# Optimization experiments

Hardware: AMD Instinct MI355X
Metric: run time of the kernel (lower is better)

## Reference

```python
import jax, jax.numpy as jnp
import numpy as np

WS = 16
NB = 800
THRESH = 0.05


def setup_inputs() -> dict:
    key = jax.random.key(0)
    k1, k2, k3, k4 = jax.random.split(key, 4)
    tensor_msi = jax.random.uniform(k1, (1, 64, 512, 512), dtype=jnp.float32)
    tensor_he = jax.random.uniform(k2, (1, 3, 512, 512), dtype=jnp.float32)
    i_idx = jax.random.randint(k3, (NB,), 0, 512 - WS, dtype=jnp.int32)
    j_idx = jax.random.randint(k4, (NB,), 0, 512 - WS, dtype=jnp.int32)
    return {
        "tensor_msi": tensor_msi,
        "tensor_he": tensor_he,
        "i_idx": i_idx,
        "j_idx": j_idx,
        "window_size": WS,
        "batch": NB,
    }


def reference(tensor_msi, tensor_he, i_idx, j_idx, window_size, batch):
    u = tensor_msi.shape[1]
    msi = tensor_msi[:, : u // 2]  # only first half of MSI channels is used
    ws = window_size
    p = ws * ws

    def get_patch(x, i, j):
        # x: [1, C, M, N] -> [C, ws*ws]
        c = x.shape[1]
        patch = jax.lax.dynamic_slice(x, (0, 0, i, j), (1, c, ws, ws))
        return patch.reshape(c, p)

    def pdist2(x, mask):
        # pairwise squared L2 distance over positions: D[a,b] = sum_k (x[k,a]-x[k,b])^2
        sq = jnp.sum(x * x, axis=0)  # [p]
        gram = jnp.einsum("kp,kq->pq", x, x)  # [p, p]
        d = sq[:, None] + sq[None, :] - 2.0 * gram
        # zero out rows/cols where the HE patch intensity sum < THRESH
        return d * mask[:, None] * mask[None, :]

    def per_patch(i, j):
        pm = get_patch(msi, i, j)  # [u//2, p]
        ph = get_patch(tensor_he, i, j)  # [3, p]
        # NOTE: original code computes index_zero from MSI then overwrites it
        # with the HE-based one; only the HE mask is applied to both.
        mask = (jnp.sum(ph, axis=0) >= THRESH).astype(pm.dtype)  # [p]
        dm = pdist2(pm, mask)
        dh = jax.lax.stop_gradient(pdist2(ph, mask))  # .detach()
        return jnp.mean(jnp.abs(dm - dh))  # L1Loss mean

    losses = jax.vmap(per_patch)(i_idx, j_idx)  # [batch]
    return jnp.sum(losses) / (batch // 5)
```

## Files before the change

### kernel.cpp

```cpp
#include <hip/hip_runtime.h>
#include <hip/hip_bf16.h>


#define PSZ  256
#define IMG  512
#define IMG2 (IMG * IMG)
#define XSTR 40

typedef __attribute__((ext_vector_type(8))) short short8;
typedef __attribute__((ext_vector_type(4))) float float4v;

static __device__ __forceinline__ unsigned short f2bf(float v) {
    union { __hip_bfloat16 b; unsigned short u; } cv;
    cv.b = __float2bfloat16(v);
    return cv.u;
}
static __device__ __forceinline__ float bf2f(unsigned short u) {
    union { unsigned int u; float f; } cv;
    cv.u = ((unsigned int)u) << 16;
    return cv.f;
}

__global__ __launch_bounds__(256, 4)
void corr_loss_kernel(const float* __restrict__ msi,
                      const float* __restrict__ he,
                      const int* __restrict__ i_idx,
                      const int* __restrict__ j_idx,
                      float* __restrict__ partial)
{
    __shared__ __align__(16) unsigned short xs[PSZ * XSTR];
    __shared__ __align__(16) unsigned short eA[PSZ * 8];
    __shared__ __align__(16) unsigned short eB[PSZ * 8];
    __shared__ float red[4];

    const int b = blockIdx.x;
    const int t = threadIdx.x;
    const int i0 = i_idx[b], j0 = j_idx[b];

    {
        const int r = t >> 4, c = t & 15;
        const float* hp = he + (size_t)(i0 + r) * IMG + (j0 + c);
        const float* mp = msi + (size_t)(i0 + r) * IMG + (j0 + c);

        float h0 = hp[0], h1 = hp[IMG2], h2 = hp[2 * IMG2];
        float v[32];
#pragma unroll
        for (int ch = 0; ch < 32; ++ch) v[ch] = mp[(size_t)ch * IMG2];

        const float mf = (h0 + h1 + h2 >= 0.05f) ? 1.f : 0.f;
        const unsigned short hb0 = f2bf(h0 * mf), hb1 = f2bf(h1 * mf), hb2 = f2bf(h2 * mf);
        const float hr0 = bf2f(hb0), hr1 = bf2f(hb1), hr2 = bf2f(hb2);
        const float sh = hr0 * hr0 + hr1 * hr1 + hr2 * hr2;

        float sm = 0.f;
#pragma unroll
        for (int g = 0; g < 4; ++g) {
            unsigned int pk[4];
#pragma unroll
            for (int k = 0; k < 4; ++k) {
                unsigned short lo = f2bf(v[g * 8 + 2 * k]     * mf);
                unsigned short hi = f2bf(v[g * 8 + 2 * k + 1] * mf);
                float fl = bf2f(lo), fh = bf2f(hi);
                sm = fmaf(fl, fl, sm);
                sm = fmaf(fh, fh, sm);
                pk[k] = (unsigned int)lo | ((unsigned int)hi << 16);
            }
            *(uint4*)&xs[t * XSTR + g * 8] = make_uint4(pk[0], pk[1], pk[2], pk[3]);
        }
        const float s = sm - sh;
        const unsigned short shi = f2bf(s);
        const unsigned short slo = f2bf(s - bf2f(shi));
        const unsigned short mb  = (mf != 0.f) ? (unsigned short)0x3F80 : (unsigned short)0;
        const unsigned short d0  = f2bf(2.f * hr0);
        const unsigned short d1  = f2bf(2.f * hr1);
        const unsigned short d2  = f2bf(2.f * hr2);
        *(uint4*)&eA[t * 8] = make_uint4(
            (unsigned)d0 | ((unsigned)d1 << 16),
            (unsigned)d2 | ((unsigned)shi << 16),
            (unsigned)slo | ((unsigned)mb << 16),
            (unsigned)mb);
        *(uint4*)&eB[t * 8] = make_uint4(
            (unsigned)hb0 | ((unsigned)hb1 << 16),
            (unsigned)hb2 | ((unsigned)mb << 16),
            (unsigned)mb | ((unsigned)shi << 16),
            (unsigned)slo);
    }
    __syncthreads();

    const int lane = t & 63, w = t >> 6;
    const int mrow = lane & 15, quad = lane >> 4;
    const short8 zfrag = {0, 0, 0, 0, 0, 0, 0, 0};

    short8 Am[4], Ah[4];
#pragma unroll
    for (int ii = 0; ii < 4; ++ii) {
        const int ri = ((w << 2) + ii) * 16 + mrow;
        uint4 u = *(const uint4*)&xs[ri * XSTR + (quad << 3)];
        u.x = (u.x ^ 0x80008000u) + 0x00800080u;
        u.y = (u.y ^ 0x80008000u) + 0x00800080u;
        u.z = (u.z ^ 0x80008000u) + 0x00800080u;
        u.w = (u.w ^ 0x80008000u) + 0x00800080u;
        Am[ii] = *(const short8*)&u;
        Ah[ii] = (quad == 0) ? *(const short8*)&eA[ri << 3] : zfrag;
    }

    float acc[4] = {0.f, 0.f, 0.f, 0.f};
#pragma unroll 4
    for (int j = 0; j < 16; ++j) {
        const int cj = (j << 4) + mrow;
        short8 Bm = *(const short8*)&xs[cj * XSTR + (quad << 3)];
        short8 Bh = (quad == 0) ? *(const short8*)&eB[cj << 3] : zfrag;
        float4v g[4];
#pragma unroll
        for (int ii = 0; ii < 4; ++ii) {
            g[ii] = (float4v){0.f, 0.f, 0.f, 0.f};
            g[ii] = __builtin_amdgcn_mfma_f32_16x16x32_bf16(Ah[ii], Bh, g[ii], 0, 0, 0);
            g[ii] = __builtin_amdgcn_mfma_f32_16x16x32_bf16(Am[ii], Bm, g[ii], 0, 0, 0);
        }
#pragma unroll
        for (int ii = 0; ii < 4; ++ii) {
            acc[ii] += fabsf(g[ii][0]);
            acc[ii] += fabsf(g[ii][1]);
            acc[ii] += fabsf(g[ii][2]);
            acc[ii] += fabsf(g[ii][3]);
        }
    }
    float a = (acc[0] + acc[1]) + (acc[2] + acc[3]);

#pragma unroll
    for (int off = 32; off > 0; off >>= 1)
        a += __shfl_down(a, off, 64);
    if (lane == 0) red[w] = a;
    __syncthreads();
    if (t == 0)
        partial[b] = (red[0] + red[1]) + (red[2] + red[3]);
}

__global__ __launch_bounds__(256)
void reduce_kernel(const float* __restrict__ partial, float* __restrict__ out,
                   int n, float scale)
{
    __shared__ float red[4];
    float a = 0.f;
    for (int i = threadIdx.x; i < n; i += 256) a += partial[i];
#pragma unroll
    for (int off = 32; off > 0; off >>= 1)
        a += __shfl_down(a, off, 64);
    const int lane = threadIdx.x & 63, w = threadIdx.x >> 6;
    if (lane == 0) red[w] = a;
    __syncthreads();
    if (threadIdx.x == 0)
        out[0] = ((red[0] + red[1]) + (red[2] + red[3])) * scale;
}

extern "C" void kernel_launch(void* const* d_in, const int* in_sizes, int n_in,
                              void* d_out, int out_size, void* d_ws, size_t ws_size,
                              hipStream_t stream) {
    const float* msi   = (const float*)d_in[0];
    const float* he    = (const float*)d_in[1];
    const int*   i_idx = (const int*)d_in[2];
    const int*   j_idx = (const int*)d_in[3];
    const int    NB    = in_sizes[2];
    float*       out   = (float*)d_out;
    float*       part  = (float*)d_ws;

    const float scale = 1.0f / ((float)(PSZ * PSZ) * (float)(NB / 5));
    corr_loss_kernel<<<NB, 256, 0, stream>>>(msi, he, i_idx, j_idx, part);
    reduce_kernel<<<1, 256, 0, stream>>>(part, out, NB, scale);
}
```

Measured before the change: 109.8 us.

## Exploit distance-matrix symmetry with 32x32 MFMA tiles and balanced triangular work

Switches from 16x16x32 to 32x32x16 bf16 MFMA tiles and computes only the upper-triangular block pairs of the symmetric 256x256 difference matrix. Off-diagonal blocks are counted twice and diagonal blocks once. Each wave pairs block rows w and 7-w so every wave does the same amount of work. This roughly halves the MFMA and abs-sum work, but adds branches inside the loop and changes the summation order.

```diff
diff --git a/kernel.cpp b/kernel.cpp
--- a/kernel.cpp
+++ b/kernel.cpp
@@ -8,7 +8,7 @@
 #define XSTR 40
 
 typedef __attribute__((ext_vector_type(8))) short short8;
-typedef __attribute__((ext_vector_type(4))) float float4v;
+typedef __attribute__((ext_vector_type(16))) float f32x16;
 
 static __device__ __forceinline__ unsigned short f2bf(float v) {
     union { __hip_bfloat16 b; unsigned short u; } cv;
@@ -19,6 +19,28 @@
     union { unsigned int u; float f; } cv;
     cv.u = ((unsigned int)u) << 16;
     return cv.f;
+}
+
+static __device__ __forceinline__ short8 neg2(uint4 u) {
+    u.x = (u.x ^ 0x80008000u) + 0x00800080u;
+    u.y = (u.y ^ 0x80008000u) + 0x00800080u;
+    u.z = (u.z ^ 0x80008000u) + 0x00800080u;
+    u.w = (u.w ^ 0x80008000u) + 0x00800080u;
+    return *(short8*)&u;
+}
+
+static __device__ __forceinline__ float abs_sum16(f32x16 g) {
+    float s0 = fabsf(g[0])  + fabsf(g[1]);
+    float s1 = fabsf(g[2])  + fabsf(g[3]);
+    float s2 = fabsf(g[4])  + fabsf(g[5]);
+    float s3 = fabsf(g[6])  + fabsf(g[7]);
+    float s4 = fabsf(g[8])  + fabsf(g[9]);
+    float s5 = fabsf(g[10]) + fabsf(g[11]);
+    float s6 = fabsf(g[12]) + fabsf(g[13]);
+    float s7 = fabsf(g[14]) + fabsf(g[15]);
+    s0 += s1; s2 += s3; s4 += s5; s6 += s7;
+    s0 += s2; s4 += s6;
+    return s0 + s4;
 }
 
 __global__ __launch_bounds__(256, 4)
@@ -88,44 +110,46 @@
     __syncthreads();
 
     const int lane = t & 63, w = t >> 6;
-    const int mrow = lane & 15, quad = lane >> 4;
+    const int row = lane & 31, half = lane >> 5;
+    const int rA = w, rB = 7 - w;
     const short8 zfrag = {0, 0, 0, 0, 0, 0, 0, 0};
+    const f32x16 zacc = {0.f, 0.f, 0.f, 0.f, 0.f, 0.f, 0.f, 0.f,
+                         0.f, 0.f, 0.f, 0.f, 0.f, 0.f, 0.f, 0.f};
 
-    short8 Am[4], Ah[4];
+    const int gA = (rA << 5) + row;
+    const int gB = (rB << 5) + row;
+    const short8 AmA0 = neg2(*(const uint4*)&xs[gA * XSTR + (half << 3)]);
+    const short8 AmA1 = neg2(*(const uint4*)&xs[gA * XSTR + 16 + (half << 3)]);
+    const short8 AhA  = half ? zfrag : *(const short8*)&eA[gA << 3];
+    const short8 AmB0 = neg2(*(const uint4*)&xs[gB * XSTR + (half << 3)]);
+    const short8 AmB1 = neg2(*(const uint4*)&xs[gB * XSTR + 16 + (half << 3)]);
+    const short8 AhB  = half ? zfrag : *(const short8*)&eA[gB << 3];
+
+    float acc1 = 0.f;
+    float acc2 = 0.f;
 #pragma unroll
-    for (int ii = 0; ii < 4; ++ii) {
-        const int ri = ((w << 2) + ii) * 16 + mrow;
-        uint4 u = *(const uint4*)&xs[ri * XSTR + (quad << 3)];
-        u.x = (u.x ^ 0x80008000u) + 0x00800080u;
-        u.y = (u.y ^ 0x80008000u) + 0x00800080u;
-        u.z = (u.z ^ 0x80008000u) + 0x00800080u;
-        u.w = (u.w ^ 0x80008000u) + 0x00800080u;
-        Am[ii] = *(const short8*)&u;
-        Ah[ii] = (quad == 0) ? *(const short8*)&eA[ri << 3] : zfrag;
-    }
+    for (int j = 0; j < 8; ++j) {
+        if (j < rA) continue;
+        const int gC = (j << 5) + row;
+        const short8 Bm0 = *(const short8*)&xs[gC * XSTR + (half << 3)];
+        const short8 Bm1 = *(const short8*)&xs[gC * XSTR + 16 + (half << 3)];
+        const short8 Bh  = half ? zfrag : *(const short8*)&eB[gC << 3];
 
-    float acc[4] = {0.f, 0.f, 0.f, 0.f};
-#pragma unroll 4
-    for (int j = 0; j < 16; ++j) {
-        const int cj = (j << 4) + mrow;
-        short8 Bm = *(const short8*)&xs[cj * XSTR + (quad << 3)];
-        short8 Bh = (quad == 0) ? *(const short8*)&eB[cj << 3] : zfrag;
-        float4v g[4];
-#pragma unroll
-        for (int ii = 0; ii < 4; ++ii) {
-            g[ii] = (float4v){0.f, 0.f, 0.f, 0.f};
-            g[ii] = __builtin_amdgcn_mfma_f32_16x16x32_bf16(Ah[ii], Bh, g[ii], 0, 0, 0);
-            g[ii] = __builtin_amdgcn_mfma_f32_16x16x32_bf16(Am[ii], Bm, g[ii], 0, 0, 0);
-        }
-#pragma unroll
-        for (int ii = 0; ii < 4; ++ii) {
-            acc[ii] += fabsf(g[ii][0]);
-            acc[ii] += fabsf(g[ii][1]);
-            acc[ii] += fabsf(g[ii][2]);
-            acc[ii] += fabsf(g[ii][3]);
+        f32x16 g = __builtin_amdgcn_mfma_f32_32x32x16_bf16(AhA,  Bh,  zacc, 0, 0, 0);
+        g = __builtin_amdgcn_mfma_f32_32x32x16_bf16(AmA0, Bm0, g, 0, 0, 0);
+        g = __builtin_amdgcn_mfma_f32_32x32x16_bf16(AmA1, Bm1, g, 0, 0, 0);
+        const float s = abs_sum16(g);
+        if (j == rA) acc1 += s; else acc2 += s;
+
+        if (j >= rB) {
+            f32x16 h = __builtin_amdgcn_mfma_f32_32x32x16_bf16(AhB,  Bh,  zacc, 0, 0, 0);
+            h = __builtin_amdgcn_mfma_f32_32x32x16_bf16(AmB0, Bm0, h, 0, 0, 0);
+            h = __builtin_amdgcn_mfma_f32_32x32x16_bf16(AmB1, Bm1, h, 0, 0, 0);
+            const float s2 = abs_sum16(h);
+            if (j == rB) acc1 += s2; else acc2 += s2;
         }
     }
-    float a = (acc[0] + acc[1]) + (acc[2] + acc[3]);
+    float a = acc1 + 2.f * acc2;
 
 #pragma unroll
     for (int off = 32; off > 0; off >>= 1)
```

Result: faster. 106.5 us, median of 2 (-3.0%).
